# Optimization experiments

Hardware: AMD Instinct MI355X
Metric: run time of the kernel (lower is better)

Reference implementation:

```python
import jax, jax.numpy as jnp
import numpy as np

D_MODEL = 1024
N_HEADS = 16
D_K = D_MODEL // N_HEADS
D_FF = 4096
B, S = 4, 2048
EPS = 1e-5


def setup_inputs() -> dict:
    key = jax.random.key(0)
    ks = jax.random.split(key, 16)
    s = 0.02
    inp = {
        'x': jax.random.normal(ks[0], (B, S, D_MODEL), dtype=jnp.float32),
        'Wq': jax.random.normal(ks[1], (D_MODEL, D_MODEL), dtype=jnp.float32) * s,
        'bq': jnp.zeros((D_MODEL,), jnp.float32),
        'Wk': jax.random.normal(ks[2], (D_MODEL, D_MODEL), dtype=jnp.float32) * s,
        'bk': jnp.zeros((D_MODEL,), jnp.float32),
        'Wv': jax.random.normal(ks[3], (D_MODEL, D_MODEL), dtype=jnp.float32) * s,
        'bv': jnp.zeros((D_MODEL,), jnp.float32),
        'Wo': jax.random.normal(ks[4], (D_MODEL, D_MODEL), dtype=jnp.float32) * s,
        'bo': jnp.zeros((D_MODEL,), jnp.float32),
        'W1': jax.random.normal(ks[5], (D_MODEL, D_FF), dtype=jnp.float32) * s,
        'b1': jnp.zeros((D_FF,), jnp.float32),
        'W2': jax.random.normal(ks[6], (D_FF, D_MODEL), dtype=jnp.float32) * s,
        'b2': jnp.zeros((D_MODEL,), jnp.float32),
        'g1': jnp.ones((D_MODEL,), jnp.float32),
        'be1': jnp.zeros((D_MODEL,), jnp.float32),
        'g2': jnp.ones((D_MODEL,), jnp.float32),
        'be2': jnp.zeros((D_MODEL,), jnp.float32),
    }
    return inp


def _layernorm(x, g, b):
    mu = jnp.mean(x, axis=-1, keepdims=True)
    var = jnp.var(x, axis=-1, keepdims=True)
    return (x - mu) * jax.lax.rsqrt(var + EPS) * g + b


def reference(x, Wq, bq, Wk, bk, Wv, bv, Wo, bo, W1, b1, W2, b2, g1, be1, g2, be2):
    # Multi-head self-attention (mask=None, dropout in eval -> identity)
    q = (x @ Wq + bq).reshape(B, S, N_HEADS, D_K).transpose(0, 2, 1, 3)  # [B,H,S,Dk]
    k = (x @ Wk + bk).reshape(B, S, N_HEADS, D_K).transpose(0, 2, 1, 3)
    v = (x @ Wv + bv).reshape(B, S, N_HEADS, D_K).transpose(0, 2, 1, 3)
    scores = jnp.einsum('bhqd,bhkd->bhqk', q, k) / jnp.sqrt(jnp.float32(D_K))
    attn = jax.nn.softmax(scores, axis=-1)
    out = jnp.einsum('bhqk,bhkd->bhqd', attn, v)          # [B,H,S,Dk]
    out = out.transpose(0, 2, 1, 3).reshape(B, S, D_MODEL)
    att_out = out @ Wo + bo
    x2 = _layernorm(x + att_out, g1, be1)
    ff = jax.nn.relu(x2 @ W1 + b1) @ W2 + b2
    return _layernorm(x2 + ff, g2, be2)
```

## Files before the change

kernel.cpp:

```cpp
#include <hip/hip_runtime.h>
#include <hip/hip_bf16.h>

typedef __attribute__((ext_vector_type(8)))  __bf16 bf16x8;
typedef __attribute__((ext_vector_type(4)))  float  f32x4;
typedef __attribute__((ext_vector_type(16))) float  f32x16;

static __device__ __forceinline__ unsigned short f2bf(float x) {
    unsigned int u = __float_as_uint(x);
    unsigned int r = (u + 0x7FFFu + ((u >> 16) & 1u)) >> 16;
    return (unsigned short)r;
}
static __device__ __forceinline__ float bf2f(unsigned short u) {
    return __uint_as_float(((unsigned int)u) << 16);
}

static __device__ __forceinline__ float fast_exp2(float x) {
    float r;
    asm("v_exp_f32 %0, %1" : "=v"(r) : "v"(x));
    return r;
}
static __device__ __forceinline__ unsigned int cvt_pk_bf16(float a, float b) {
    unsigned int r;
    asm("v_cvt_pk_bf16_f32 %0, %1, %2" : "=v"(r) : "v"(a), "v"(b));
    return r;
}

static __device__ __forceinline__ void gload_lds16(const ushort* g, ushort* l) {
    __builtin_amdgcn_global_load_lds((const __attribute__((address_space(1))) void*)g,
                                     (__attribute__((address_space(3))) void*)l, 16, 0, 0);
}

static __device__ __forceinline__ void barrier_fence() {
    __builtin_amdgcn_s_barrier();
    __builtin_amdgcn_sched_barrier(0);
    asm volatile("" ::: "memory");
}

static __device__ __forceinline__ int xcd_swz(int id, int nwg) {
    return (id & 7) * (nwg >> 3) + (id >> 3);
}

__global__ __launch_bounds__(256) void cast_bf16_kernel(const float* __restrict__ in,
                                                        ushort* __restrict__ out, int n4) {
    int i = blockIdx.x * 256 + threadIdx.x;
    if (i < n4) {
        float4 v = reinterpret_cast<const float4*>(in)[i];
        ushort4 o;
        o.x = f2bf(v.x); o.y = f2bf(v.y); o.z = f2bf(v.z); o.w = f2bf(v.w);
        reinterpret_cast<ushort4*>(out)[i] = o;
    }
}

__global__ __launch_bounds__(256) void transpose_cast_kernel(const float* __restrict__ in,
                                                             ushort* __restrict__ out,
                                                             int K, int N) {
    __shared__ float tile[32][33];
    const int tx = threadIdx.x;
    const int ty = threadIdx.y;
    const int n0 = blockIdx.x * 32;
    const int k0 = blockIdx.y * 32;
    for (int i = ty; i < 32; i += 8)
        tile[i][tx] = in[(size_t)(k0 + i) * N + n0 + tx];
    __syncthreads();
    for (int i = ty; i < 32; i += 8)
        out[(size_t)(n0 + i) * K + k0 + tx] = f2bf(tile[tx][i]);
}

__global__ __launch_bounds__(256) void transpose_cast3_kernel(const float* __restrict__ w0,
                                                              const float* __restrict__ w1,
                                                              const float* __restrict__ w2,
                                                              ushort* __restrict__ out) {
    __shared__ float tile[32][33];
    const int tx = threadIdx.x;
    const int ty = threadIdx.y;
    const int n0 = blockIdx.x * 32;
    const int k0 = blockIdx.y * 32;
    const int z  = blockIdx.z;
    const float* in = (z == 0) ? w0 : (z == 1 ? w1 : w2);
    ushort* o = out + (size_t)z * 1024 * 1024;
    for (int i = ty; i < 32; i += 8)
        tile[i][tx] = in[(size_t)(k0 + i) * 1024 + n0 + tx];
    __syncthreads();
    for (int i = ty; i < 32; i += 8)
        o[(size_t)(n0 + i) * 1024 + k0 + tx] = f2bf(tile[tx][i]);
}

template<int RELU, int OUTBF, int QKV, int RES>
__global__ __launch_bounds__(256) void gemm_p3(const ushort* __restrict__ A,
                                               const ushort* __restrict__ Bt,
                                               const float* __restrict__ b0,
                                               const float* __restrict__ b1_,
                                               const float* __restrict__ b2_,
                                               const void* __restrict__ xres,
                                               void* __restrict__ Cp,
                                               int M, int N, int K) {
    __shared__ ushort As[3][4096];
    __shared__ ushort Bs[3][4096];
    const int tid  = threadIdx.x;
    const int lane = tid & 63;
    const int w    = tid >> 6;
    const int wr   = w >> 1, wc = w & 1;
    const int nwg = gridDim.x * gridDim.y;
    int wid = xcd_swz(blockIdx.y * gridDim.x + blockIdx.x, nwg);
    const int bx = wid % gridDim.x;
    const int by = wid / gridDim.x;
    const int m0 = by * 128;
    const int n0 = bx * 128;
    const int lr = lane & 15;
    const int lg = lane >> 4;
    const int xc = (lg ^ ((lr >> 1) & 3)) * 8;

    const int r0 = w * 32 + (lane >> 2);
    const int c8 = ((lane & 3) ^ ((lane >> 3) & 3)) * 8;
    const ushort* gA0 = A  + (size_t)(m0 + r0)      * K + c8;
    const ushort* gA1 = A  + (size_t)(m0 + r0 + 16) * K + c8;
    const ushort* gB0 = Bt + (size_t)(n0 + r0)      * K + c8;
    const ushort* gB1 = Bt + (size_t)(n0 + r0 + 16) * K + c8;
    const int wb = w * 1024;

    f32x4 acc[4][4];
    const f32x4 z = {0.f, 0.f, 0.f, 0.f};
#pragma unroll
    for (int i = 0; i < 4; i++)
#pragma unroll
        for (int j = 0; j < 4; j++) acc[i][j] = z;

    const int nt = K >> 5;

#pragma unroll
    for (int t = 0; t < 2; ++t) {
        const int kn = t * 32;
        gload_lds16(gA0 + kn, &As[t][wb]);
        gload_lds16(gA1 + kn, &As[t][wb + 512]);
        gload_lds16(gB0 + kn, &Bs[t][wb]);
        gload_lds16(gB1 + kn, &Bs[t][wb + 512]);
    }

    int cur = 0;
    for (int t = 0; t < nt; ++t) {
        if (t + 1 < nt) asm volatile("s_waitcnt vmcnt(4)" ::: "memory");
        else            asm volatile("s_waitcnt vmcnt(0)" ::: "memory");
        barrier_fence();

        if (t + 2 < nt) {
            const int bi = (cur + 2 >= 3) ? cur - 1 : cur + 2;
            const int kn = (t + 2) * 32;
            gload_lds16(gA0 + kn, &As[bi][wb]);
            gload_lds16(gA1 + kn, &As[bi][wb + 512]);
            gload_lds16(gB0 + kn, &Bs[bi][wb]);
            gload_lds16(gB1 + kn, &Bs[bi][wb + 512]);
        }

        const ushort* Asb = As[cur];
        const ushort* Bsb = Bs[cur];
        bf16x8 af[4], bfr[4];
#pragma unroll
        for (int i = 0; i < 4; i++)
            af[i] = *reinterpret_cast<const bf16x8*>(&Asb[(wr * 64 + i * 16 + lr) * 32 + xc]);
#pragma unroll
        for (int j = 0; j < 4; j++)
            bfr[j] = *reinterpret_cast<const bf16x8*>(&Bsb[(wc * 64 + j * 16 + lr) * 32 + xc]);
#pragma unroll
        for (int i = 0; i < 4; i++)
#pragma unroll
            for (int j = 0; j < 4; j++)
                acc[i][j] = __builtin_amdgcn_mfma_f32_16x16x32_bf16(af[i], bfr[j], acc[i][j], 0, 0, 0);

        cur = (cur == 2) ? 0 : cur + 1;
    }

    const float* bias;
    float qscale = 1.0f;
    if (QKV) {
        bias = (n0 < 1024) ? b0 : (n0 < 2048 ? b1_ : b2_);
        if (n0 < 1024) qscale = 0.18033688f;
    } else {
        bias = b0;
    }
    const int nb = QKV ? (n0 & 1023) : n0;
    const int rbase = (lane >> 4) * 4;
#pragma unroll
    for (int i = 0; i < 4; i++) {
#pragma unroll
        for (int j = 0; j < 4; j++) {
            const int cloc = wc * 64 + j * 16 + lr;
            const float bv = bias[nb + cloc];
#pragma unroll
            for (int r = 0; r < 4; r++) {
                const int row = m0 + wr * 64 + i * 16 + rbase + r;
                float v = acc[i][j][r] + bv;
                if (RES == 1) v += ((const float*)xres)[(size_t)row * N + n0 + cloc];
                if (RES == 2) v += bf2f(((const ushort*)xres)[(size_t)row * N + n0 + cloc]);
                if (RELU) v = v > 0.f ? v : 0.f;
                if (QKV)  v *= qscale;
                if (OUTBF) ((ushort*)Cp)[(size_t)row * N + n0 + cloc] = f2bf(v);
                else       ((float*)Cp)[(size_t)row * N + n0 + cloc] = v;
            }
        }
    }
}

#define ASWZ(row, col) ((row) * 64 + ((col) ^ ((((row) ^ ((row) >> 3)) & 7) << 3)))

__global__ __launch_bounds__(256, 3) void attn_kernel(const ushort* __restrict__ QKV,
                                                      ushort* __restrict__ O) {
    __shared__ ushort Ks[2][4096];
    __shared__ ushort Vt[2][4096];
    const int tid  = threadIdx.x;
    const int lane = tid & 63;
    const int w    = tid >> 6;
    const int l31  = lane & 31;
    const int hi   = lane >> 5;

    int blk = xcd_swz(blockIdx.x, gridDim.x);
    const int qb = blk & 15;
    const int h  = (blk >> 4) & 15;
    const int b  = blk >> 8;
    const int s0 = qb * 128 + w * 32;
    const size_t rowb   = (size_t)b * 2048;
    const size_t base_q = rowb * 3072 + (size_t)h * 64;
    const size_t base_k = base_q + 1024;
    const size_t base_v = base_q + 2048;
    const size_t base_o = rowb * 1024 + (size_t)h * 64;

    bf16x8 qf[4];
#pragma unroll
    for (int ks = 0; ks < 4; ks++)
        qf[ks] = *reinterpret_cast<const bf16x8*>(
            &QKV[base_q + (size_t)(s0 + l31) * 3072 + ks * 16 + 8 * hi]);

    int off8[2][4];
#pragma unroll
    for (int sub = 0; sub < 2; sub++)
#pragma unroll
        for (int ks = 0; ks < 4; ks++)
            off8[sub][ks] = ASWZ(sub * 32 + l31, ks * 16 + 8 * hi);

    const int tS2 = tid >> 3;
    const int ccS = tid & 7;
    int voff[8];
#pragma unroll
    for (int jj = 0; jj < 8; jj++)
        voff[jj] = ASWZ(ccS * 8 + jj, 2 * tS2);
    const int tk1 = tS2 + 32;
    const int sz0 = (tS2 ^ (tS2 >> 3)) & 7;
    const int sz1 = (tk1 ^ (tk1 >> 3)) & 7;
    const ushort* pK0 = QKV + base_k + (size_t)tS2 * 3072 + (ccS ^ sz0) * 8;
    const ushort* pK1 = QKV + base_k + (size_t)tk1 * 3072 + (ccS ^ sz1) * 8;
    const ushort* pV0 = QKV + base_v + (size_t)(2 * tS2)     * 3072 + ccS * 8;
    const ushort* pV1 = QKV + base_v + (size_t)(2 * tS2 + 1) * 3072 + ccS * 8;
    const size_t step = (size_t)64 * 3072;

    gload_lds16(pK0, &Ks[0][w * 512]);
    gload_lds16(pK1, &Ks[0][2048 + w * 512]);
    {
        int4 v0 = *reinterpret_cast<const int4*>(pV0);
        int4 v1 = *reinterpret_cast<const int4*>(pV1);
        const ushort* vs0 = reinterpret_cast<const ushort*>(&v0);
        const ushort* vs1 = reinterpret_cast<const ushort*>(&v1);
#pragma unroll
        for (int jj = 0; jj < 8; jj++)
            *reinterpret_cast<unsigned*>(&Vt[0][voff[jj]]) =
                (unsigned)vs0[jj] | ((unsigned)vs1[jj] << 16);
    }
    pK0 += step; pK1 += step; pV0 += step; pV1 += step;
    __syncthreads();

    f32x16 oacc0, oacc1;
    for (int i = 0; i < 16; i++) { oacc0[i] = 0.f; oacc1[i] = 0.f; }
    float lacc = 0.f;
    int cur = 0;

    for (int it = 0; it < 32; ++it) {
        int4 nv0, nv1;
        if (it < 31) {
            gload_lds16(pK0, &Ks[cur ^ 1][w * 512]);
            gload_lds16(pK1, &Ks[cur ^ 1][2048 + w * 512]);
            nv0 = *reinterpret_cast<const int4*>(pV0);
            nv1 = *reinterpret_cast<const int4*>(pV1);
            pK0 += step; pK1 += step; pV0 += step; pV1 += step;
        }

        f32x16 sa0, sa1;
        for (int i = 0; i < 16; i++) { sa0[i] = 0.f; sa1[i] = 0.f; }
        __builtin_amdgcn_s_setprio(1);
#pragma unroll
        for (int ks = 0; ks < 4; ks++) {
            bf16x8 k0 = *reinterpret_cast<const bf16x8*>(&Ks[cur][off8[0][ks]]);
            sa0 = __builtin_amdgcn_mfma_f32_32x32x16_bf16(k0, qf[ks], sa0, 0, 0, 0);
        }
#pragma unroll
        for (int ks = 0; ks < 4; ks++) {
            bf16x8 k1 = *reinterpret_cast<const bf16x8*>(&Ks[cur][off8[1][ks]]);
            sa1 = __builtin_amdgcn_mfma_f32_32x32x16_bf16(k1, qf[ks], sa1, 0, 0, 0);
        }
        __builtin_amdgcn_s_setprio(0);

        unsigned pk0[8], pk1[8];
#pragma unroll
        for (int i = 0; i < 8; i++) {
            float plo = fast_exp2(sa0[2 * i]);
            float phi = fast_exp2(sa0[2 * i + 1]);
            lacc += plo + phi;
            pk0[i] = cvt_pk_bf16(plo, phi);
        }
#pragma unroll
        for (int i = 0; i < 8; i++) {
            float plo = fast_exp2(sa1[2 * i]);
            float phi = fast_exp2(sa1[2 * i + 1]);
            lacc += plo + phi;
            pk1[i] = cvt_pk_bf16(plo, phi);
        }

        __builtin_amdgcn_s_setprio(1);
#pragma unroll
        for (int ks = 0; ks < 4; ks++) {
            const int bi = 4 * (ks & 1);
            unsigned a, bb, c, d;
            if (ks < 2) { a = pk0[bi]; bb = pk0[bi + 1]; c = pk0[bi + 2]; d = pk0[bi + 3]; }
            else        { a = pk1[bi]; bb = pk1[bi + 1]; c = pk1[bi + 2]; d = pk1[bi + 3]; }
            asm("v_permlane32_swap_b32 %0, %1" : "+v"(a), "+v"(c));
            asm("v_permlane32_swap_b32 %0, %1" : "+v"(bb), "+v"(d));
            union { unsigned u[4]; bf16x8 v; } fr;
            fr.u[0] = a; fr.u[1] = bb; fr.u[2] = c; fr.u[3] = d;
            bf16x8 v0 = *reinterpret_cast<const bf16x8*>(&Vt[cur][off8[0][ks]]);
            oacc0 = __builtin_amdgcn_mfma_f32_32x32x16_bf16(fr.v, v0, oacc0, 0, 0, 0);
            bf16x8 v1 = *reinterpret_cast<const bf16x8*>(&Vt[cur][off8[1][ks]]);
            oacc1 = __builtin_amdgcn_mfma_f32_32x32x16_bf16(fr.v, v1, oacc1, 0, 0, 0);
        }
        __builtin_amdgcn_s_setprio(0);

        if (it < 31) {
            const ushort* vs0 = reinterpret_cast<const ushort*>(&nv0);
            const ushort* vs1 = reinterpret_cast<const ushort*>(&nv1);
#pragma unroll
            for (int jj = 0; jj < 8; jj++)
                *reinterpret_cast<unsigned*>(&Vt[cur ^ 1][voff[jj]]) =
                    (unsigned)vs0[jj] | ((unsigned)vs1[jj] << 16);
        }
        __syncthreads();
        cur ^= 1;
    }

    const float ltot = lacc + __shfl_xor(lacc, 32);
    const float inv  = 1.f / ltot;
#pragma unroll
    for (int r = 0; r < 16; r++) {
        const int qloc = (r & 3) + 8 * (r >> 2) + 4 * hi;
        const float invq = __shfl(inv, qloc);
        const size_t rowoff = base_o + (size_t)(s0 + qloc) * 1024 + l31;
        O[rowoff]      = f2bf(oacc0[r] * invq);
        O[rowoff + 32] = f2bf(oacc1[r] * invq);
    }
}

template<int OUTBF>
__global__ __launch_bounds__(256) void ln_one(const ushort* __restrict__ zin,
                                              const float* __restrict__ g,
                                              const float* __restrict__ be,
                                              void* __restrict__ out) {
    const int row = blockIdx.x;
    const int tid = threadIdx.x;
    const ushort4 zv = reinterpret_cast<const ushort4*>(zin + (size_t)row * 1024)[tid];
    float v[4] = {bf2f(zv.x), bf2f(zv.y), bf2f(zv.z), bf2f(zv.w)};
    float s  = v[0] + v[1] + v[2] + v[3];
    float s2 = v[0]*v[0] + v[1]*v[1] + v[2]*v[2] + v[3]*v[3];
    for (int off = 32; off; off >>= 1) { s += __shfl_down(s, off); s2 += __shfl_down(s2, off); }
    __shared__ float red[8];
    const int w = tid >> 6, lane = tid & 63;
    if (lane == 0) { red[w] = s; red[4 + w] = s2; }
    __syncthreads();
    if (tid == 0) {
        const float ts  = red[0] + red[1] + red[2] + red[3];
        const float ts2 = red[4] + red[5] + red[6] + red[7];
        const float mu  = ts * (1.f / 1024.f);
        const float var = ts2 * (1.f / 1024.f) - mu * mu;
        red[0] = mu;
        red[1] = rsqrtf(var + 1e-5f);
    }
    __syncthreads();
    const float mu = red[0], rs = red[1];
    const float4 gv = reinterpret_cast<const float4*>(g)[tid];
    const float4 bv = reinterpret_cast<const float4*>(be)[tid];
    float o0 = (v[0] - mu) * rs * gv.x + bv.x;
    float o1 = (v[1] - mu) * rs * gv.y + bv.y;
    float o2 = (v[2] - mu) * rs * gv.z + bv.z;
    float o3 = (v[3] - mu) * rs * gv.w + bv.w;
    if (OUTBF) {
        ushort4 ob;
        ob.x = f2bf(o0); ob.y = f2bf(o1); ob.z = f2bf(o2); ob.w = f2bf(o3);
        reinterpret_cast<ushort4*>((ushort*)out + (size_t)row * 1024)[tid] = ob;
    } else {
        float4 of;
        of.x = o0; of.y = o1; of.z = o2; of.w = o3;
        reinterpret_cast<float4*>((float*)out + (size_t)row * 1024)[tid] = of;
    }
}

extern "C" void kernel_launch(void* const* d_in, const int* in_sizes, int n_in,
                              void* d_out, int out_size, void* d_ws, size_t ws_size,
                              hipStream_t stream) {
    const float* x  = (const float*)d_in[0];
    const float* Wq = (const float*)d_in[1];  const float* bq = (const float*)d_in[2];
    const float* Wk = (const float*)d_in[3];  const float* bk = (const float*)d_in[4];
    const float* Wv = (const float*)d_in[5];  const float* bv = (const float*)d_in[6];
    const float* Wo = (const float*)d_in[7];  const float* bo = (const float*)d_in[8];
    const float* W1 = (const float*)d_in[9];  const float* b1 = (const float*)d_in[10];
    const float* W2 = (const float*)d_in[11]; const float* b2 = (const float*)d_in[12];
    const float* g1 = (const float*)d_in[13]; const float* be1 = (const float*)d_in[14];
    const float* g2 = (const float*)d_in[15]; const float* be2 = (const float*)d_in[16];

    char* ws = (char*)d_ws;
    const size_t MBy = (size_t)1 << 20;
    ushort* xb    = (ushort*)(ws + 0 * MBy);
    ushort* wqkvT = (ushort*)(ws + 16 * MBy);
    ushort* woT   = (ushort*)(ws + 22 * MBy);
    ushort* w1T   = (ushort*)(ws + 24 * MBy);
    ushort* w2T   = (ushort*)(ws + 32 * MBy);
    ushort* QKVb  = (ushort*)(ws + 40 * MBy);
    ushort* AOb   = (ushort*)(ws + 88 * MBy);
    ushort* h1    = (ushort*)(ws + 40 * MBy);
    ushort* z1b   = (ushort*)(ws + 104 * MBy);
    ushort* z2b   = (ushort*)(ws + 104 * MBy);
    ushort* x2b   = (ushort*)(ws + 120 * MBy);
    (void)ws_size; (void)n_in; (void)in_sizes; (void)out_size;

    const int M = 8192;

    cast_bf16_kernel<<<(M * 1024 / 4 + 255) / 256, 256, 0, stream>>>(x, xb, M * 1024 / 4);
    dim3 tb(32, 8);
    transpose_cast3_kernel<<<dim3(32, 32, 3), tb, 0, stream>>>(Wq, Wk, Wv, wqkvT);
    transpose_cast_kernel<<<dim3(32, 32),  tb, 0, stream>>>(Wo, woT, 1024, 1024);
    transpose_cast_kernel<<<dim3(128, 32), tb, 0, stream>>>(W1, w1T, 1024, 4096);
    transpose_cast_kernel<<<dim3(32, 128), tb, 0, stream>>>(W2, w2T, 4096, 1024);

    gemm_p3<0, 1, 1, 0><<<dim3(24, 64), 256, 0, stream>>>(xb, wqkvT, bq, bk, bv, nullptr,
                                                          QKVb, M, 3072, 1024);

    attn_kernel<<<1024, 256, 0, stream>>>(QKVb, AOb);

    gemm_p3<0, 1, 0, 1><<<dim3(8, 64), 256, 0, stream>>>(AOb, woT, bo, nullptr, nullptr, x,
                                                         z1b, M, 1024, 1024);

    ln_one<1><<<M, 256, 0, stream>>>(z1b, g1, be1, x2b);

    gemm_p3<1, 1, 0, 0><<<dim3(32, 64), 256, 0, stream>>>(x2b, w1T, b1, nullptr, nullptr,
                                                          nullptr, h1, M, 4096, 1024);
    gemm_p3<0, 1, 0, 2><<<dim3(8, 64), 256, 0, stream>>>(h1, w2T, b2, nullptr, nullptr, x2b,
                                                         z2b, M, 1024, 4096);

    ln_one<0><<<M, 256, 0, stream>>>(z2b, g2, be2, (float*)d_out);
}
```

Baseline: 402.3 us.

## Add 256x128-tile 512-thread GEMM for output projection and FFN layers

Adds a new GEMM kernel with 8 waves per block and a 256x128 output tile, double-buffered LDS loads split into two halves interleaved with MFMA phases, and barriers between MFMA groups. It replaces the previous 128-row tile kernel for the Wo, W1 and W2 GEMMs. The aim is more reuse of each B tile per block and better overlap of global-to-LDS loads with compute. The cost is one block per CU, extra barriers per K step, and fewer blocks in flight for the N=1024 GEMMs (256 blocks).

```diff
diff --git a/kernel.cpp b/kernel.cpp
--- a/kernel.cpp
+++ b/kernel.cpp
@@ -200,6 +200,173 @@
     }
 }
 
+template<int RELU, int OUTBF, int RES>
+__global__ __launch_bounds__(512, 1) void gemm_4p(const ushort* __restrict__ A,
+                                                  const ushort* __restrict__ Bt,
+                                                  const float* __restrict__ bias,
+                                                  const void* __restrict__ xres,
+                                                  void* __restrict__ Cp,
+                                                  int M, int N, int K) {
+    __shared__ ushort As[2][16384];
+    __shared__ ushort Bs[2][8192];
+    const int tid  = threadIdx.x;
+    const int lane = tid & 63;
+    const int w    = tid >> 6;
+    const int wr   = w >> 1;
+    const int wc   = w & 1;
+    const int nwg  = gridDim.x * gridDim.y;
+    int wid = xcd_swz(blockIdx.y * gridDim.x + blockIdx.x, nwg);
+    const int bx = wid % gridDim.x;
+    const int by = wid / gridDim.x;
+    const int m0 = by * 256;
+    const int n0 = bx * 128;
+    const int lr = lane & 15;
+    const int lg = lane >> 4;
+
+    int offA[4][2], offB[4][2];
+#pragma unroll
+    for (int i = 0; i < 4; i++) {
+        const int row = wr * 64 + i * 16 + lr;
+#pragma unroll
+        for (int kh = 0; kh < 2; kh++)
+            offA[i][kh] = row * 64 + (((kh * 4 + lg) ^ (lr & 7)) << 3);
+    }
+#pragma unroll
+    for (int j = 0; j < 4; j++) {
+        const int row = wc * 64 + j * 16 + lr;
+#pragma unroll
+        for (int kh = 0; kh < 2; kh++)
+            offB[j][kh] = row * 64 + (((kh * 4 + lg) ^ (lr & 7)) << 3);
+    }
+
+    const int srcc = ((lane & 7) ^ (lane >> 3)) * 8;
+    const ushort* gA[2][2];
+    int ldsA[2][2];
+#pragma unroll
+    for (int h = 0; h < 2; h++)
+#pragma unroll
+        for (int l = 0; l < 2; l++) {
+            const int row = h * 128 + l * 64 + w * 8 + (lane >> 3);
+            gA[h][l]  = A + (size_t)(m0 + row) * K + srcc;
+            ldsA[h][l] = h * 8192 + l * 4096 + w * 512;
+        }
+    const ushort* gB[2];
+    int ldsB[2];
+#pragma unroll
+    for (int h = 0; h < 2; h++) {
+        const int row = h * 64 + w * 8 + (lane >> 3);
+        gB[h]  = Bt + (size_t)(n0 + row) * K + srcc;
+        ldsB[h] = h * 4096 + w * 512;
+    }
+
+    f32x4 acc[4][4];
+    const f32x4 z = {0.f, 0.f, 0.f, 0.f};
+#pragma unroll
+    for (int i = 0; i < 4; i++)
+#pragma unroll
+        for (int j = 0; j < 4; j++) acc[i][j] = z;
+
+    const int nt = K >> 6;
+
+#pragma unroll
+    for (int h = 0; h < 2; h++) {
+        gload_lds16(gA[h][0], &As[0][ldsA[h][0]]);
+        gload_lds16(gA[h][1], &As[0][ldsA[h][1]]);
+        gload_lds16(gB[h],    &Bs[0][ldsB[h]]);
+    }
+
+    int cur = 0;
+    for (int t = 0; t < nt; ++t) {
+        const int kn = (t + 1) << 6;
+        if (t + 1 < nt) {
+            gload_lds16(gA[0][0] + kn, &As[cur ^ 1][ldsA[0][0]]);
+            gload_lds16(gA[0][1] + kn, &As[cur ^ 1][ldsA[0][1]]);
+            gload_lds16(gB[0]    + kn, &Bs[cur ^ 1][ldsB[0]]);
+            asm volatile("s_waitcnt vmcnt(3)" ::: "memory");
+        } else {
+            asm volatile("s_waitcnt vmcnt(0)" ::: "memory");
+        }
+        barrier_fence();
+        {
+            const ushort* Asb = As[cur];
+            const ushort* Bsb = Bs[cur];
+            bf16x8 b0[4], a0, a1;
+#pragma unroll
+            for (int j = 0; j < 4; j++)
+                b0[j] = *reinterpret_cast<const bf16x8*>(&Bsb[offB[j][0]]);
+            a0 = *reinterpret_cast<const bf16x8*>(&Asb[offA[0][0]]);
+            a1 = *reinterpret_cast<const bf16x8*>(&Asb[offA[1][0]]);
+            __builtin_amdgcn_s_setprio(1);
+#pragma unroll
+            for (int j = 0; j < 4; j++) {
+                acc[0][j] = __builtin_amdgcn_mfma_f32_16x16x32_bf16(a0, b0[j], acc[0][j], 0, 0, 0);
+                acc[1][j] = __builtin_amdgcn_mfma_f32_16x16x32_bf16(a1, b0[j], acc[1][j], 0, 0, 0);
+            }
+            __builtin_amdgcn_s_setprio(0);
+            barrier_fence();
+            a0 = *reinterpret_cast<const bf16x8*>(&Asb[offA[2][0]]);
+            a1 = *reinterpret_cast<const bf16x8*>(&Asb[offA[3][0]]);
+            __builtin_amdgcn_s_setprio(1);
+#pragma unroll
+            for (int j = 0; j < 4; j++) {
+                acc[2][j] = __builtin_amdgcn_mfma_f32_16x16x32_bf16(a0, b0[j], acc[2][j], 0, 0, 0);
+                acc[3][j] = __builtin_amdgcn_mfma_f32_16x16x32_bf16(a1, b0[j], acc[3][j], 0, 0, 0);
+            }
+            __builtin_amdgcn_s_setprio(0);
+            barrier_fence();
+            if (t + 1 < nt) {
+                gload_lds16(gA[1][0] + kn, &As[cur ^ 1][ldsA[1][0]]);
+                gload_lds16(gA[1][1] + kn, &As[cur ^ 1][ldsA[1][1]]);
+                gload_lds16(gB[1]    + kn, &Bs[cur ^ 1][ldsB[1]]);
+            }
+#pragma unroll
+            for (int j = 0; j < 4; j++)
+                b0[j] = *reinterpret_cast<const bf16x8*>(&Bsb[offB[j][1]]);
+            a0 = *reinterpret_cast<const bf16x8*>(&Asb[offA[0][1]]);
+            a1 = *reinterpret_cast<const bf16x8*>(&Asb[offA[1][1]]);
+            __builtin_amdgcn_s_setprio(1);
+#pragma unroll
+            for (int j = 0; j < 4; j++) {
+                acc[0][j] = __builtin_amdgcn_mfma_f32_16x16x32_bf16(a0, b0[j], acc[0][j], 0, 0, 0);
+                acc[1][j] = __builtin_amdgcn_mfma_f32_16x16x32_bf16(a1, b0[j], acc[1][j], 0, 0, 0);
+            }
+            __builtin_amdgcn_s_setprio(0);
+            barrier_fence();
+            a0 = *reinterpret_cast<const bf16x8*>(&Asb[offA[2][1]]);
+            a1 = *reinterpret_cast<const bf16x8*>(&Asb[offA[3][1]]);
+            __builtin_amdgcn_s_setprio(1);
+#pragma unroll
+            for (int j = 0; j < 4; j++) {
+                acc[2][j] = __builtin_amdgcn_mfma_f32_16x16x32_bf16(a0, b0[j], acc[2][j], 0, 0, 0);
+                acc[3][j] = __builtin_amdgcn_mfma_f32_16x16x32_bf16(a1, b0[j], acc[3][j], 0, 0, 0);
+            }
+            __builtin_amdgcn_s_setprio(0);
+            barrier_fence();
+        }
+        cur ^= 1;
+    }
+
+    const int rbase = (lane >> 4) * 4;
+#pragma unroll
+    for (int i = 0; i < 4; i++) {
+#pragma unroll
+        for (int j = 0; j < 4; j++) {
+            const int cloc = wc * 64 + j * 16 + lr;
+            const float bv = bias[n0 + cloc];
+#pragma unroll
+            for (int r = 0; r < 4; r++) {
+                const int row = m0 + wr * 64 + i * 16 + rbase + r;
+                float v = acc[i][j][r] + bv;
+                if (RES == 1) v += ((const float*)xres)[(size_t)row * N + n0 + cloc];
+                if (RES == 2) v += bf2f(((const ushort*)xres)[(size_t)row * N + n0 + cloc]);
+                if (RELU) v = v > 0.f ? v : 0.f;
+                if (OUTBF) ((ushort*)Cp)[(size_t)row * N + n0 + cloc] = f2bf(v);
+                else       ((float*)Cp)[(size_t)row * N + n0 + cloc] = v;
+            }
+        }
+    }
+}
+
 #define ASWZ(row, col) ((row) * 64 + ((col) ^ ((((row) ^ ((row) >> 3)) & 7) << 3)))
 
 __global__ __launch_bounds__(256, 3) void attn_kernel(const ushort* __restrict__ QKV,
@@ -439,15 +606,14 @@
 
     attn_kernel<<<1024, 256, 0, stream>>>(QKVb, AOb);
 
-    gemm_p3<0, 1, 0, 1><<<dim3(8, 64), 256, 0, stream>>>(AOb, woT, bo, nullptr, nullptr, x,
-                                                         z1b, M, 1024, 1024);
+    gemm_4p<0, 1, 1><<<dim3(8, 32), 512, 0, stream>>>(AOb, woT, bo, x, z1b, M, 1024, 1024);
 
     ln_one<1><<<M, 256, 0, stream>>>(z1b, g1, be1, x2b);
 
-    gemm_p3<1, 1, 0, 0><<<dim3(32, 64), 256, 0, stream>>>(x2b, w1T, b1, nullptr, nullptr,
-                                                          nullptr, h1, M, 4096, 1024);
-    gemm_p3<0, 1, 0, 2><<<dim3(8, 64), 256, 0, stream>>>(h1, w2T, b2, nullptr, nullptr, x2b,
-                                                         z2b, M, 1024, 4096);
+    gemm_4p<1, 1, 0><<<dim3(32, 32), 512, 0, stream>>>(x2b, w1T, b1, nullptr, h1,
+                                                       M, 4096, 1024);
+    gemm_4p<0, 1, 2><<<dim3(8, 32), 512, 0, stream>>>(h1, w2T, b2, x2b, z2b,
+                                                      M, 1024, 4096);
 
     ln_one<0><<<M, 256, 0, stream>>>(z2b, g2, be2, (float*)d_out);
 }
```

Measured after the change: 464.8 us. 1.16x slower.

## Use 512-thread attention blocks with 8 waves sharing each K/V tile

Applied to the files above, without the earlier changes.

Doubles the attention block to 8 waves covering 256 query rows, so each K/V tile loaded into shared memory serves twice as many queries. The grid halves, and each thread now loads one K row and one V row instead of two, with the V transpose writing single 16-bit elements. This cuts global K/V traffic per query and the cooperative load work per thread. In exchange it adds more waves per barrier, uses 16-bit LDS stores with possible bank conflicts, and requests higher occupancy through launch bounds, which may pressure registers.

```diff
diff --git a/kernel.cpp b/kernel.cpp
--- a/kernel.cpp
+++ b/kernel.cpp
@@ -202,7 +202,7 @@
 
 #define ASWZ(row, col) ((row) * 64 + ((col) ^ ((((row) ^ ((row) >> 3)) & 7) << 3)))
 
-__global__ __launch_bounds__(256, 3) void attn_kernel(const ushort* __restrict__ QKV,
+__global__ __launch_bounds__(512, 4) void attn_kernel(const ushort* __restrict__ QKV,
                                                       ushort* __restrict__ O) {
     __shared__ ushort Ks[2][4096];
     __shared__ ushort Vt[2][4096];
@@ -213,10 +213,10 @@
     const int hi   = lane >> 5;
 
     int blk = xcd_swz(blockIdx.x, gridDim.x);
-    const int qb = blk & 15;
-    const int h  = (blk >> 4) & 15;
-    const int b  = blk >> 8;
-    const int s0 = qb * 128 + w * 32;
+    const int qb = blk & 7;
+    const int h  = (blk >> 3) & 15;
+    const int b  = blk >> 7;
+    const int s0 = qb * 256 + w * 32;
     const size_t rowb   = (size_t)b * 2048;
     const size_t base_q = rowb * 3072 + (size_t)h * 64;
     const size_t base_k = base_q + 1024;
@@ -236,34 +236,25 @@
         for (int ks = 0; ks < 4; ks++)
             off8[sub][ks] = ASWZ(sub * 32 + l31, ks * 16 + 8 * hi);
 
-    const int tS2 = tid >> 3;
+    const int tS  = tid >> 3;
     const int ccS = tid & 7;
     int voff[8];
 #pragma unroll
     for (int jj = 0; jj < 8; jj++)
-        voff[jj] = ASWZ(ccS * 8 + jj, 2 * tS2);
-    const int tk1 = tS2 + 32;
-    const int sz0 = (tS2 ^ (tS2 >> 3)) & 7;
-    const int sz1 = (tk1 ^ (tk1 >> 3)) & 7;
-    const ushort* pK0 = QKV + base_k + (size_t)tS2 * 3072 + (ccS ^ sz0) * 8;
-    const ushort* pK1 = QKV + base_k + (size_t)tk1 * 3072 + (ccS ^ sz1) * 8;
-    const ushort* pV0 = QKV + base_v + (size_t)(2 * tS2)     * 3072 + ccS * 8;
-    const ushort* pV1 = QKV + base_v + (size_t)(2 * tS2 + 1) * 3072 + ccS * 8;
+        voff[jj] = ASWZ(ccS * 8 + jj, tS);
+    const int szK = (tS ^ (tS >> 3)) & 7;
+    const ushort* pK = QKV + base_k + (size_t)tS * 3072 + (ccS ^ szK) * 8;
+    const ushort* pV = QKV + base_v + (size_t)tS * 3072 + ccS * 8;
     const size_t step = (size_t)64 * 3072;
 
-    gload_lds16(pK0, &Ks[0][w * 512]);
-    gload_lds16(pK1, &Ks[0][2048 + w * 512]);
+    gload_lds16(pK, &Ks[0][w * 512]);
     {
-        int4 v0 = *reinterpret_cast<const int4*>(pV0);
-        int4 v1 = *reinterpret_cast<const int4*>(pV1);
-        const ushort* vs0 = reinterpret_cast<const ushort*>(&v0);
-        const ushort* vs1 = reinterpret_cast<const ushort*>(&v1);
-#pragma unroll
-        for (int jj = 0; jj < 8; jj++)
-            *reinterpret_cast<unsigned*>(&Vt[0][voff[jj]]) =
-                (unsigned)vs0[jj] | ((unsigned)vs1[jj] << 16);
-    }
-    pK0 += step; pK1 += step; pV0 += step; pV1 += step;
+        int4 v0 = *reinterpret_cast<const int4*>(pV);
+        const ushort* vs = reinterpret_cast<const ushort*>(&v0);
+#pragma unroll
+        for (int jj = 0; jj < 8; jj++) Vt[0][voff[jj]] = vs[jj];
+    }
+    pK += step; pV += step;
     __syncthreads();
 
     f32x16 oacc0, oacc1;
@@ -272,13 +263,11 @@
     int cur = 0;
 
     for (int it = 0; it < 32; ++it) {
-        int4 nv0, nv1;
+        int4 nv;
         if (it < 31) {
-            gload_lds16(pK0, &Ks[cur ^ 1][w * 512]);
-            gload_lds16(pK1, &Ks[cur ^ 1][2048 + w * 512]);
-            nv0 = *reinterpret_cast<const int4*>(pV0);
-            nv1 = *reinterpret_cast<const int4*>(pV1);
-            pK0 += step; pK1 += step; pV0 += step; pV1 += step;
+            gload_lds16(pK, &Ks[cur ^ 1][w * 512]);
+            nv = *reinterpret_cast<const int4*>(pV);
+            pK += step; pV += step;
         }
 
         f32x16 sa0, sa1;
@@ -331,12 +320,9 @@
         __builtin_amdgcn_s_setprio(0);
 
         if (it < 31) {
-            const ushort* vs0 = reinterpret_cast<const ushort*>(&nv0);
-            const ushort* vs1 = reinterpret_cast<const ushort*>(&nv1);
-#pragma unroll
-            for (int jj = 0; jj < 8; jj++)
-                *reinterpret_cast<unsigned*>(&Vt[cur ^ 1][voff[jj]]) =
-                    (unsigned)vs0[jj] | ((unsigned)vs1[jj] << 16);
+            const ushort* vs = reinterpret_cast<const ushort*>(&nv);
+#pragma unroll
+            for (int jj = 0; jj < 8; jj++) Vt[cur ^ 1][voff[jj]] = vs[jj];
         }
         __syncthreads();
         cur ^= 1;
@@ -437,7 +423,7 @@
     gemm_p3<0, 1, 1, 0><<<dim3(24, 64), 256, 0, stream>>>(xb, wqkvT, bq, bk, bv, nullptr,
                                                           QKVb, M, 3072, 1024);
 
-    attn_kernel<<<1024, 256, 0, stream>>>(QKVb, AOb);
+    attn_kernel<<<512, 512, 0, stream>>>(QKVb, AOb);
 
     gemm_p3<0, 1, 0, 1><<<dim3(8, 64), 256, 0, stream>>>(AOb, woT, bo, nullptr, nullptr, x,
                                                          z1b, M, 1024, 1024);
```

New measurement: 397.9 us. Within noise of the previous version (-1.1%).
